# Optimization experiments

Hardware: AMD Instinct MI355X
Metric: run time of the kernel (lower is better)

Reference implementation:

```python
import jax, jax.numpy as jnp
import numpy as np
from jax import lax


def _conv(x, W, b):
    # x: [B,C,H,W], W: [O,I,3,3] -> [B,O,H,W], SAME padding, stride 1
    y = lax.conv_general_dilated(x, W, window_strides=(1, 1), padding='SAME',
                                 dimension_numbers=('NCHW', 'OIHW', 'NCHW'))
    return y + b[None, :, None, None]


def _cell(x, h, c, W, b):
    # Standard ConvLSTMCell: conv(concat(x,h)) -> 4*Hd gate channels (i,f,o,g)
    gates = _conv(jnp.concatenate([x, h], axis=1), W, b)
    ci, cf, co, cg = jnp.split(gates, 4, axis=1)
    i = jax.nn.sigmoid(ci)
    f = jax.nn.sigmoid(cf)
    o = jax.nn.sigmoid(co)
    g = jnp.tanh(cg)
    c_next = f * c + i * g
    h_next = o * jnp.tanh(c_next)
    return h_next, c_next


def setup_inputs() -> dict:
    key = jax.random.key(0)
    ks = jax.random.split(key, 4)
    B, T, C, H, W = 1, 32, 4, 128, 128
    Hd = 64
    x = jax.random.normal(ks[0], (B, T, C, H, W), dtype=jnp.float32)
    # small init scale to keep sigmoid/tanh out of deep saturation
    W0 = jax.random.normal(ks[1], (4 * Hd, C + Hd, 3, 3), dtype=jnp.float32) * 0.05
    b0 = jnp.zeros((4 * Hd,), dtype=jnp.float32)
    W1 = jax.random.normal(ks[2], (4 * Hd, Hd + Hd, 3, 3), dtype=jnp.float32) * 0.05
    b1 = jnp.zeros((4 * Hd,), dtype=jnp.float32)
    Wr = jax.random.normal(ks[3], (1, Hd, 3, 3), dtype=jnp.float32) * 0.05
    br = jnp.zeros((1,), dtype=jnp.float32)
    return {"x": x, "W0": W0, "b0": b0, "W1": W1, "b1": b1, "Wr": Wr, "br": br}


def reference(x, W0, b0, W1, b1, Wr, br):
    # Train mode with epsilon=1 (deterministic teacher forcing), hidden_state=None
    B, T, C, H, Wd = x.shape
    Hd = Wr.shape[1]
    zeros = jnp.zeros((B, Hd, H, Wd), dtype=x.dtype)
    carry0 = (zeros, zeros, zeros, zeros)  # (h0, c0, h1, c1)

    def step(carry, x_t):
        h0, c0, h1, c1 = carry
        h0, c0 = _cell(x_t, h0, c0, W0, b0)
        h1, c1 = _cell(h0, h1, c1, W1, b1)
        y = _conv(h1, Wr, br)  # [B,1,H,W]
        return (h0, c0, h1, c1), y[0]  # squeeze batch dim (B=1) -> [1,H,W]

    xs = jnp.transpose(x, (1, 0, 2, 3, 4))  # [T,B,C,H,W]
    _, ys = lax.scan(step, carry0, xs)
    return ys  # [T,1,H,W]
```

## Files before the change

kernel.cpp:

```cpp
#include <hip/hip_runtime.h>
#include <cstdint>
#include <cmath>

#define HW 128
#define NPIX (HW * HW)

typedef _Float16 half8 __attribute__((ext_vector_type(8)));
typedef _Float16 half4 __attribute__((ext_vector_type(4)));
typedef float floatx16 __attribute__((ext_vector_type(16)));
typedef unsigned long long u64;

__device__ __forceinline__ float sigf(float x) {
    return __builtin_amdgcn_rcpf(1.0f + __expf(-x));
}
__device__ __forceinline__ float tanhf_(float x) {
    float cx = fminf(fmaxf(x, -20.0f), 20.0f);
    float e2 = __expf(2.0f * cx);
    return (e2 - 1.0f) * __builtin_amdgcn_rcpf(e2 + 1.0f);
}

__device__ __forceinline__ half8 ld_coh(const _Float16* p) {
    union { u64 u[2]; half8 h; } cv;
    cv.u[0] = __hip_atomic_load((const u64*)p,
                                __ATOMIC_RELAXED, __HIP_MEMORY_SCOPE_AGENT);
    cv.u[1] = __hip_atomic_load((const u64*)p + 1,
                                __ATOMIC_RELAXED, __HIP_MEMORY_SCOPE_AGENT);
    return cv.h;
}

__device__ __forceinline__ void st_coh8(_Float16* p, half4 v) {
    asm volatile("global_store_dwordx2 %0, %1, off sc0 sc1"
                 :: "v"(p), "v"(v) : "memory");
}
__device__ __forceinline__ void st_coh4(float* p, float v) {
    asm volatile("global_store_dword %0, %1, off sc0 sc1"
                 :: "v"(p), "v"(v) : "memory");
}

__device__ __forceinline__ void group_sync(unsigned* gcnt, int g,
                                           int gy, int gx, unsigned k)
{
    asm volatile("s_waitcnt vmcnt(0)" ::: "memory");
    __syncthreads();
    const int tid = threadIdx.x;
    if (tid == 0)
        __hip_atomic_fetch_add(gcnt + g * 16, 1u,
                               __ATOMIC_RELAXED, __HIP_MEMORY_SCOPE_AGENT);
    if (tid < 9) {
        int dy = tid / 3 - 1, dx = tid % 3 - 1;
        int gy2 = gy + dy, gx2 = gx + dx;
        if (gy2 >= 0 && gy2 < 8 && gx2 >= 0 && gx2 < 4) {
            const unsigned* p = gcnt + (gy2 * 4 + gx2) * 16;
            while (__hip_atomic_load(p, __ATOMIC_RELAXED,
                                     __HIP_MEMORY_SCOPE_AGENT) < 8u * k)
                __builtin_amdgcn_s_sleep(1);
        }
    }
    __syncthreads();
}

template<int NKC, int CELL>
__device__ __forceinline__ void cell_phase(
    const _Float16* __restrict__ xt,
    const _Float16* __restrict__ hA,
    const _Float16* __restrict__ hB,
    const _Float16* wlds,
    const float* blds,
    float (&cr)[4],
    _Float16* __restrict__ hOut,
    _Float16* sbuf,
    const int (&spb)[2], const int (&slo)[2], int ch16,
    int y0, int x0, int s)
{
    const int tid  = threadIdx.x;
    const int lane = tid & 63;
    const int w    = tid >> 6;
    const int cl   = lane & 31;
    const int l5   = lane >> 5;

    half8 vv[2];
    auto stage_load = [&](int kc) {
        #pragma unroll
        for (int e0 = 0; e0 < 2; ++e0) {
            half8 v = {0, 0, 0, 0, 0, 0, 0, 0};
            const int pb = spb[e0];
            if (pb >= 0) {
                if (CELL == 0) {
                    if (kc == 0) { if (ch16 == 0) v = *(const half8*)(xt + (pb >> 3)); }
                    else v = ld_coh(hA + pb + (kc - 1) * 16);
                } else {
                    v = (kc < 4) ? ld_coh(hA + pb + kc * 16)
                                 : ld_coh(hB + pb + (kc - 4) * 16);
                }
            }
            vv[e0] = v;
        }
    };
    auto stage_write = [&](int b) {
        #pragma unroll
        for (int e0 = 0; e0 < 2; ++e0)
            if (slo[e0] >= 0) *(half8*)(sbuf + b * 9792 + slo[e0]) = vv[e0];
    };

    floatx16 acc;
    #pragma unroll
    for (int i = 0; i < 16; ++i) acc[i] = 0.0f;

    __syncthreads();
    stage_load(0);
    stage_write(0);
    __syncthreads();

    #pragma unroll 1
    for (int kc = 0; kc < NKC; ++kc) {
        if (kc + 1 < NKC) stage_load(kc + 1);
        const _Float16* wk = wlds + (size_t)(kc * 9) * 512 + lane * 8;
        const _Float16* bbase = sbuf + ((kc & 1) * 2 + l5) * 4896;
        #pragma unroll
        for (int dy = 0; dy < 3; ++dy)
            #pragma unroll
            for (int dx = 0; dx < 3; ++dx) {
                half8 a = *(const half8*)(wk + (dy * 3 + dx) * 512);
                half8 b = *(const half8*)(bbase + ((w + dy) * 34 + cl + dx) * 8);
                acc = __builtin_amdgcn_mfma_f32_32x32x16_f16(a, b, acc, 0, 0, 0);
            }
        if (kc + 1 < NKC) stage_write((kc + 1) & 1);
        __syncthreads();
    }

    const int px = (y0 + w) * HW + x0 + cl;
    half4 hn;
    #pragma unroll
    for (int j = 0; j < 4; ++j) {
        const int bo = CELL * 32 + 4 * l5 + j;
        float iv = sigf(acc[     j] + blds[bo]);
        float fv = sigf(acc[ 4 + j] + blds[bo + 8]);
        float ov = sigf(acc[ 8 + j] + blds[bo + 16]);
        float gv = tanhf_(acc[12 + j] + blds[bo + 24]);
        float cv = fv * cr[j] + iv * gv;
        cr[j] = cv;
        hn[j] = (_Float16)(ov * tanhf_(cv));
    }
    st_coh8(hOut + (size_t)px * 64 + s * 8 + 4 * l5, hn);
}

__device__ __forceinline__ void readout_phase(
    half8 rv, const float* wl, float brv,
    float* __restrict__ yout, _Float16* sbuf, int rlo, int yidx)
{
    const int tid = threadIdx.x;
    __syncthreads();
    if (rlo >= 0) *(half8*)(sbuf + rlo) = rv;
    __syncthreads();

    if (tid < 512) {
        const int sub = tid & 7;
        const int p   = tid >> 3;
        const int pr  = p >> 3, pcc = p & 7;
        float sacc = 0.0f;
        #pragma unroll
        for (int dy = 0; dy < 3; ++dy)
            #pragma unroll
            for (int dx = 0; dx < 3; ++dx) {
                int pc = (pr + dy) * 10 + (pcc + dx);
                half8 hv = *(const half8*)(sbuf + ((size_t)pc * 8 + sub) * 8);
                int tap = dy * 3 + dx;
                #pragma unroll
                for (int j = 0; j < 8; ++j)
                    sacc += wl[(sub * 8 + j) * 9 + tap] * (float)hv[j];
            }
        sacc += __shfl_xor(sacc, 1);
        sacc += __shfl_xor(sacc, 2);
        sacc += __shfl_xor(sacc, 4);
        if (sub == 0) st_coh4(yout + yidx, sacc + brv);
    }
}

__global__ __launch_bounds__(1024, 4)
void mega(const _Float16* __restrict__ xh, const _Float16* __restrict__ WpG,
          const float* __restrict__ b0g, const float* __restrict__ b1g,
          const float* __restrict__ Wr, const float* __restrict__ br,
          _Float16* __restrict__ h0a, _Float16* __restrict__ h0b,
          _Float16* __restrict__ h1a, _Float16* __restrict__ h1b,
          float* __restrict__ y, unsigned* gcnt)
{
    extern __shared__ __align__(16) char dyn[];
    _Float16* wlds = (_Float16*)dyn;
    _Float16* sbuf = (_Float16*)(dyn + 119808);
    float*    wl   = (float*)(dyn + 158976);
    float*    blds = (float*)(dyn + 161280);

    const int tid = threadIdx.x;
    const int bid = blockIdx.x;
    const int s = bid >> 5, g = bid & 31;
    const int ggy = g >> 2, ggx = g & 3;
    const int y0 = ggy * 16, x0 = ggx * 32;

    const half8* wsrc = (const half8*)(WpG + (size_t)s * 59904);
    for (int i = tid; i < 7488; i += 1024) ((half8*)wlds)[i] = wsrc[i];
    for (int i = tid; i < 576; i += 1024) wl[i] = Wr[i];
    if (tid < 64) {
        int cell = tid >> 5, gj = tid & 31;
        int gate = gj >> 3, h8 = gj & 7;
        blds[tid] = (cell ? b1g : b0g)[gate * 64 + s * 8 + h8];
    }
    const float brv = br[0];
    float c0r[4] = {0, 0, 0, 0};
    float c1r[4] = {0, 0, 0, 0};

    const int ch16 = tid & 1;
    int spb[2], slo[2];
    #pragma unroll
    for (int e0 = 0; e0 < 2; ++e0) {
        int e = tid + e0 * 1024;
        spb[e0] = -1; slo[e0] = -1;
        if (e < 1224) {
            int pc = e >> 1;
            int r = pc / 34, c = pc - r * 34;
            int gy = y0 - 1 + r, gx = x0 - 1 + c;
            slo[e0] = (ch16 * 612 + pc) * 8;
            if (gy >= 0 && gy < HW && gx >= 0 && gx < HW)
                spb[e0] = (gy * HW + gx) * 64 + ch16 * 8;
        }
    }
    const int ch8 = tid & 7;
    const int py0 = y0 + (s >> 2) * 8, px0 = x0 + (s & 3) * 8;
    int rpb = -1, rlo = -1;
    if (tid < 800) {
        int pc = tid >> 3;
        int r = pc / 10, c = pc - r * 10;
        int gy = py0 - 1 + r, gx = px0 - 1 + c;
        rlo = (pc * 8 + ch8) * 8;
        if (gy >= 0 && gy < HW && gx >= 0 && gx < HW)
            rpb = (gy * HW + gx) * 64 + ch8 * 8;
    }
    const int yidx = (py0 + ((tid >> 3) >> 3)) * HW + px0 + ((tid >> 3) & 7);

    __syncthreads();

    #pragma unroll 1
    for (int t = 0; t < 32; ++t) {
        const _Float16* xt = xh + (size_t)t * NPIX * 8;
        const _Float16* h0r = (t & 1) ? h0b : h0a;
        _Float16*       h0w = (t & 1) ? h0a : h0b;
        const _Float16* h1r = (t & 1) ? h1b : h1a;
        _Float16*       h1w = (t & 1) ? h1a : h1b;

        cell_phase<5, 0>(xt, h0r, nullptr, wlds, blds, c0r, h0w, sbuf,
                         spb, slo, ch16, y0, x0, s);
        group_sync(gcnt, g, ggy, ggx, (unsigned)(t + 1));

        half8 rv = {0, 0, 0, 0, 0, 0, 0, 0};
        if (t > 0 && rpb >= 0) rv = ld_coh(h1r + rpb);

        cell_phase<8, 1>(nullptr, h0w, h1r, wlds + 23040, blds, c1r, h1w, sbuf,
                         spb, slo, ch16, y0, x0, s);

        if (t > 0)
            readout_phase(rv, wl, brv, y + (size_t)(t - 1) * NPIX, sbuf,
                          rlo, yidx);
    }
    group_sync(gcnt, g, ggy, ggx, 33u);
    {
        half8 rv = {0, 0, 0, 0, 0, 0, 0, 0};
        if (rpb >= 0) rv = ld_coh(h1a + rpb);
        readout_phase(rv, wl, brv, y + (size_t)31 * NPIX, sbuf, rlo, yidx);
    }
}

__global__ void pack_w(const float* __restrict__ W, _Float16* __restrict__ Wp,
                       int NKC, int CIN_W, int cell1, int base, int total)
{
    int idx = blockIdx.x * 256 + threadIdx.x;
    if (idx >= total) return;
    int j = idx & 7, l = (idx >> 3) & 63;
    int rest = idx >> 9;
    int tap = rest % 9;
    int kt  = rest / 9;
    int kc = kt % NKC, s = kt / NKC;
    int rr = l & 31, l5 = l >> 5;
    int o = (rr >> 3) * 64 + s * 8 + (rr & 7);
    int k = kc * 16 + l5 * 8 + j;
    int cin = cell1 ? ((k < 4) ? k : ((k >= 16 && k < 80) ? k - 12 : -1)) : k;
    float v = (cin >= 0) ? W[((size_t)o * CIN_W + cin) * 9 + tap] : 0.0f;
    Wp[(size_t)s * 59904 + base + (size_t)(kc * 9 + tap) * 512 + l * 8 + j] = (_Float16)v;
}

__global__ void xconv(const float* __restrict__ x, _Float16* __restrict__ xh)
{
    int idx = blockIdx.x * 256 + threadIdx.x;
    int t = idx >> 14, px = idx & 16383;
    const float* xs = x + (size_t)t * 4 * NPIX + px;
    half8 v = {0, 0, 0, 0, 0, 0, 0, 0};
    v[0] = (_Float16)xs[0];
    v[1] = (_Float16)xs[NPIX];
    v[2] = (_Float16)xs[2 * NPIX];
    v[3] = (_Float16)xs[3 * NPIX];
    *(half8*)(xh + (size_t)idx * 8) = v;
}

extern "C" void kernel_launch(void* const* d_in, const int* in_sizes, int n_in,
                              void* d_out, int out_size, void* d_ws, size_t ws_size,
                              hipStream_t stream)
{
    const float* x  = (const float*)d_in[0];
    const float* W0 = (const float*)d_in[1];
    const float* b0 = (const float*)d_in[2];
    const float* W1 = (const float*)d_in[3];
    const float* b1 = (const float*)d_in[4];
    const float* Wr = (const float*)d_in[5];
    const float* br = (const float*)d_in[6];
    float* y = (float*)d_out;

    char* ws = (char*)d_ws;
    _Float16* h0a = (_Float16*)(ws);
    _Float16* h1a = (_Float16*)(ws + (2u << 20));
    _Float16* h0b = (_Float16*)(ws + (4u << 20));
    _Float16* h1b = (_Float16*)(ws + (6u << 20));
    _Float16* xh  = (_Float16*)(ws + (8u << 20));
    _Float16* WpG = (_Float16*)(ws + (16u << 20));
    unsigned* cnt = (unsigned*)(ws + (17u << 20));

    hipMemsetAsync(ws, 0, (4u << 20), stream);
    hipMemsetAsync(cnt, 0, 2048, stream);

    pack_w<<<dim3((184320 + 255) / 256), 256, 0, stream>>>(W0, WpG, 5, 68, 1, 0, 184320);
    pack_w<<<dim3((294912 + 255) / 256), 256, 0, stream>>>(W1, WpG, 8, 128, 0, 23040, 294912);
    xconv<<<dim3(2048), 256, 0, stream>>>(x, xh);

    hipFuncSetAttribute(reinterpret_cast<const void*>(mega),
                        hipFuncAttributeMaxDynamicSharedMemorySize, 161536);
    mega<<<dim3(256), 1024, 161536, stream>>>(xh, WpG, b0, b1, Wr, br,
                                              h0a, h0b, h1a, h1b, y, cnt);
}
```

Measured before the change: 828.5 us.

## Split K across wave halves with two rows per wave and register reuse

```diff
diff --git a/kernel.cpp b/kernel.cpp
--- a/kernel.cpp
+++ b/kernel.cpp
@@ -64,84 +64,150 @@
     const _Float16* __restrict__ xt,
     const _Float16* __restrict__ hA,
     const _Float16* __restrict__ hB,
-    const _Float16* wlds,
+    const _Float16* wcell,
     const float* blds,
-    float (&cr)[4],
+    float (&cr)[2][4],
     _Float16* __restrict__ hOut,
     _Float16* sbuf,
-    const int (&spb)[2], const int (&slo)[2], int ch16,
-    int y0, int x0, int s)
-{
-    const int tid  = threadIdx.x;
-    const int lane = tid & 63;
-    const int w    = tid >> 6;
-    const int cl   = lane & 31;
-    const int l5   = lane >> 5;
-
-    half8 vv[2];
-    auto stage_load = [&](int kc) {
+    const int (&spb)[3], const int (&slo)[3],
+    const int (&sfl)[3], const int (&sch)[3],
+    int y0, int x0, int s, int kh, int wf, int lane)
+{
+    constexpr int NK0 = (NKC + 1) / 2;
+    const int cl = lane & 31, l5 = lane >> 5;
+    const int r0 = 2 * wf;
+    const int tid = threadIdx.x;
+
+    half8 vv[3];
+    auto stage_load = [&](int j) {
         #pragma unroll
-        for (int e0 = 0; e0 < 2; ++e0) {
+        for (int e0 = 0; e0 < 3; ++e0) {
             half8 v = {0, 0, 0, 0, 0, 0, 0, 0};
-            const int pb = spb[e0];
-            if (pb >= 0) {
-                if (CELL == 0) {
-                    if (kc == 0) { if (ch16 == 0) v = *(const half8*)(xt + (pb >> 3)); }
-                    else v = ld_coh(hA + pb + (kc - 1) * 16);
-                } else {
-                    v = (kc < 4) ? ld_coh(hA + pb + kc * 16)
-                                 : ld_coh(hB + pb + (kc - 4) * 16);
+            if (slo[e0] >= 0) {
+                int kc = sfl[e0] ? (NK0 + j) : j;
+                if (kc < NKC && spb[e0] >= 0) {
+                    if (CELL == 0) {
+                        if (kc == 0) { if (sch[e0] == 0) v = *(const half8*)(xt + (spb[e0] >> 3)); }
+                        else v = ld_coh(hA + spb[e0] + (kc - 1) * 16);
+                    } else {
+                        v = (kc < 4) ? ld_coh(hA + spb[e0] + kc * 16)
+                                     : ld_coh(hB + spb[e0] + (kc - 4) * 16);
+                    }
                 }
             }
             vv[e0] = v;
         }
     };
-    auto stage_write = [&](int b) {
+    auto stage_write = [&](int j) {
         #pragma unroll
-        for (int e0 = 0; e0 < 2; ++e0)
-            if (slo[e0] >= 0) *(half8*)(sbuf + b * 9792 + slo[e0]) = vv[e0];
+        for (int e0 = 0; e0 < 3; ++e0) {
+            if (slo[e0] >= 0) {
+                int kc = sfl[e0] ? (NK0 + j) : j;
+                if (kc < NKC) *(half8*)(sbuf + slo[e0]) = vv[e0];
+            }
+        }
     };
 
-    floatx16 acc;
+    floatx16 acc[2];
     #pragma unroll
-    for (int i = 0; i < 16; ++i) acc[i] = 0.0f;
-
-    __syncthreads();
+    for (int p_ = 0; p_ < 2; ++p_)
+        #pragma unroll
+        for (int i = 0; i < 16; ++i) acc[p_][i] = 0.0f;
+
     stage_load(0);
+    __syncthreads();
     stage_write(0);
     __syncthreads();
 
-    #pragma unroll 1
-    for (int kc = 0; kc < NKC; ++kc) {
-        if (kc + 1 < NKC) stage_load(kc + 1);
-        const _Float16* wk = wlds + (size_t)(kc * 9) * 512 + lane * 8;
-        const _Float16* bbase = sbuf + ((kc & 1) * 2 + l5) * 4896;
+    const _Float16* bb = sbuf + kh * 9792 + l5 * 4896;
+
+    #pragma unroll
+    for (int j = 0; j < NK0; ++j) {
+        if (j + 1 < NK0) stage_load(j + 1);
+
+        const int kc = kh ? (NK0 + j) : j;
+        if (kc < NKC) {
+            const _Float16* wk = wcell + (size_t)(kc * 9) * 512 + lane * 8;
+            half8 bufA[3], bufB[3];
+            #pragma unroll
+            for (int d = 0; d < 3; ++d) {
+                bufA[d] = *(const half8*)(bb + ((r0    ) * 34 + cl + d) * 8);
+                bufB[d] = *(const half8*)(bb + ((r0 + 1) * 34 + cl + d) * 8);
+            }
+            #pragma unroll
+            for (int dx = 0; dx < 3; ++dx) {
+                half8 a = *(const half8*)(wk + dx * 512);
+                acc[0] = __builtin_amdgcn_mfma_f32_32x32x16_f16(a, bufA[dx], acc[0], 0, 0, 0);
+                acc[1] = __builtin_amdgcn_mfma_f32_32x32x16_f16(a, bufB[dx], acc[1], 0, 0, 0);
+            }
+            #pragma unroll
+            for (int d = 0; d < 3; ++d)
+                bufA[d] = *(const half8*)(bb + ((r0 + 2) * 34 + cl + d) * 8);
+            #pragma unroll
+            for (int dx = 0; dx < 3; ++dx) {
+                half8 a = *(const half8*)(wk + (3 + dx) * 512);
+                acc[0] = __builtin_amdgcn_mfma_f32_32x32x16_f16(a, bufB[dx], acc[0], 0, 0, 0);
+                acc[1] = __builtin_amdgcn_mfma_f32_32x32x16_f16(a, bufA[dx], acc[1], 0, 0, 0);
+            }
+            #pragma unroll
+            for (int d = 0; d < 3; ++d)
+                bufB[d] = *(const half8*)(bb + ((r0 + 3) * 34 + cl + d) * 8);
+            #pragma unroll
+            for (int dx = 0; dx < 3; ++dx) {
+                half8 a = *(const half8*)(wk + (6 + dx) * 512);
+                acc[0] = __builtin_amdgcn_mfma_f32_32x32x16_f16(a, bufA[dx], acc[0], 0, 0, 0);
+                acc[1] = __builtin_amdgcn_mfma_f32_32x32x16_f16(a, bufB[dx], acc[1], 0, 0, 0);
+            }
+        }
+        __syncthreads();
+        if (j + 1 < NK0) {
+            stage_write(j + 1);
+            __syncthreads();
+        }
+    }
+
+    float* xch = (float*)sbuf;
+    #pragma unroll
+    for (int pos = 0; pos < 2; ++pos) {
+        if (kh == 1) {
+            float* q = xch + (tid - 512) * 16;
+            #pragma unroll
+            for (int i = 0; i < 16; i += 4)
+                *(float4*)(q + i) = make_float4(acc[pos][i], acc[pos][i + 1],
+                                                acc[pos][i + 2], acc[pos][i + 3]);
+        }
+        __syncthreads();
+        if (kh == 0) {
+            const float* q = xch + tid * 16;
+            #pragma unroll
+            for (int i = 0; i < 16; i += 4) {
+                float4 p4 = *(const float4*)(q + i);
+                acc[pos][i] += p4.x; acc[pos][i + 1] += p4.y;
+                acc[pos][i + 2] += p4.z; acc[pos][i + 3] += p4.w;
+            }
+        }
+        __syncthreads();
+    }
+
+    if (kh == 0) {
         #pragma unroll
-        for (int dy = 0; dy < 3; ++dy)
-            #pragma unroll
-            for (int dx = 0; dx < 3; ++dx) {
-                half8 a = *(const half8*)(wk + (dy * 3 + dx) * 512);
-                half8 b = *(const half8*)(bbase + ((w + dy) * 34 + cl + dx) * 8);
-                acc = __builtin_amdgcn_mfma_f32_32x32x16_f16(a, b, acc, 0, 0, 0);
-            }
-        if (kc + 1 < NKC) stage_write((kc + 1) & 1);
-        __syncthreads();
-    }
-
-    const int px = (y0 + w) * HW + x0 + cl;
-    half4 hn;
-    #pragma unroll
-    for (int j = 0; j < 4; ++j) {
-        const int bo = CELL * 32 + 4 * l5 + j;
-        float iv = sigf(acc[     j] + blds[bo]);
-        float fv = sigf(acc[ 4 + j] + blds[bo + 8]);
-        float ov = sigf(acc[ 8 + j] + blds[bo + 16]);
-        float gv = tanhf_(acc[12 + j] + blds[bo + 24]);
-        float cv = fv * cr[j] + iv * gv;
-        cr[j] = cv;
-        hn[j] = (_Float16)(ov * tanhf_(cv));
-    }
-    st_coh8(hOut + (size_t)px * 64 + s * 8 + 4 * l5, hn);
+        for (int pos = 0; pos < 2; ++pos) {
+            const int px = (y0 + r0 + pos) * HW + x0 + cl;
+            half4 hn;
+            #pragma unroll
+            for (int j = 0; j < 4; ++j) {
+                const int bo = CELL * 32 + 4 * l5 + j;
+                float iv = sigf(acc[pos][     j] + blds[bo]);
+                float fv = sigf(acc[pos][ 4 + j] + blds[bo + 8]);
+                float ov = sigf(acc[pos][ 8 + j] + blds[bo + 16]);
+                float gv = tanhf_(acc[pos][12 + j] + blds[bo + 24]);
+                float cv = fv * cr[pos][j] + iv * gv;
+                cr[pos][j] = cv;
+                hn[j] = (_Float16)(ov * tanhf_(cv));
+            }
+            st_coh8(hOut + (size_t)px * 64 + s * 8 + 4 * l5, hn);
+        }
+    }
 }
 
 __device__ __forceinline__ void readout_phase(
@@ -196,31 +262,37 @@
     const int ggy = g >> 2, ggx = g & 3;
     const int y0 = ggy * 16, x0 = ggx * 32;
 
+    const int lane = tid & 63;
+    const int wv   = tid >> 6;
+    const int kh   = wv >> 3;
+    const int wf   = wv & 7;
+
     const half8* wsrc = (const half8*)(WpG + (size_t)s * 59904);
     for (int i = tid; i < 7488; i += 1024) ((half8*)wlds)[i] = wsrc[i];
     for (int i = tid; i < 576; i += 1024) wl[i] = Wr[i];
     if (tid < 64) {
         int cell = tid >> 5, gj = tid & 31;
-        int gate = gj >> 3, h8 = gj & 7;
-        blds[tid] = (cell ? b1g : b0g)[gate * 64 + s * 8 + h8];
+        blds[tid] = (cell ? b1g : b0g)[(gj >> 3) * 64 + s * 8 + (gj & 7)];
     }
     const float brv = br[0];
-    float c0r[4] = {0, 0, 0, 0};
-    float c1r[4] = {0, 0, 0, 0};
-
-    const int ch16 = tid & 1;
-    int spb[2], slo[2];
+    float c0r[2][4] = {{0, 0, 0, 0}, {0, 0, 0, 0}};
+    float c1r[2][4] = {{0, 0, 0, 0}, {0, 0, 0, 0}};
+
+    int spb[3], slo[3], sfl[3], sch[3];
     #pragma unroll
-    for (int e0 = 0; e0 < 2; ++e0) {
+    for (int e0 = 0; e0 < 3; ++e0) {
         int e = tid + e0 * 1024;
-        spb[e0] = -1; slo[e0] = -1;
-        if (e < 1224) {
-            int pc = e >> 1;
+        spb[e0] = -1; slo[e0] = -1; sfl[e0] = 0; sch[e0] = 0;
+        if (e < 2448) {
+            int f  = (e >= 1224) ? 1 : 0;
+            int es = e - f * 1224;
+            int pc = es >> 1, ch = es & 1;
             int r = pc / 34, c = pc - r * 34;
             int gy = y0 - 1 + r, gx = x0 - 1 + c;
-            slo[e0] = (ch16 * 612 + pc) * 8;
+            slo[e0] = f * 9792 + ch * 4896 + pc * 8;
+            sfl[e0] = f; sch[e0] = ch;
             if (gy >= 0 && gy < HW && gx >= 0 && gx < HW)
-                spb[e0] = (gy * HW + gx) * 64 + ch16 * 8;
+                spb[e0] = (gy * HW + gx) * 64 + ch * 8;
         }
     }
     const int ch8 = tid & 7;
@@ -247,14 +319,14 @@
         _Float16*       h1w = (t & 1) ? h1a : h1b;
 
         cell_phase<5, 0>(xt, h0r, nullptr, wlds, blds, c0r, h0w, sbuf,
-                         spb, slo, ch16, y0, x0, s);
+                         spb, slo, sfl, sch, y0, x0, s, kh, wf, lane);
         group_sync(gcnt, g, ggy, ggx, (unsigned)(t + 1));
 
         half8 rv = {0, 0, 0, 0, 0, 0, 0, 0};
         if (t > 0 && rpb >= 0) rv = ld_coh(h1r + rpb);
 
         cell_phase<8, 1>(nullptr, h0w, h1r, wlds + 23040, blds, c1r, h1w, sbuf,
-                         spb, slo, ch16, y0, x0, s);
+                         spb, slo, sfl, sch, y0, x0, s, kh, wf, lane);
 
         if (t > 0)
             readout_phase(rv, wl, brv, y + (size_t)(t - 1) * NPIX, sbuf,
```

Measured after the change: 967.9 us. +16.8%, slower.
